# Performance work log

Measured on AMD Instinct MI355X. Metric: run time of the kernel, lower is better.

Reference implementation:

```python
import jax, jax.numpy as jnp
import numpy as np
from jax import lax

B, T, D, H, Z, L = 64, 1024, 128, 512, 64, 2

def lstm_layer(x_tbd, h0, c0, Wih, Whh, bih, bhh):
    # x_tbd: [T,B,Din]; precompute input contribution (big GEMM outside scan)
    gx = jnp.einsum('tbd,gd->tbg', x_tbd, Wih) + (bih + bhh)  # [T,B,4H]
    def step(carry, gxt):
        h, c = carry
        gates = gxt + h @ Whh.T
        i, f, g, o = jnp.split(gates, 4, axis=-1)
        c = jax.nn.sigmoid(f) * c + jax.nn.sigmoid(i) * jnp.tanh(g)
        h = jax.nn.sigmoid(o) * jnp.tanh(c)
        return (h, c), h
    (hT, cT), hs = lax.scan(step, (h0, c0), gx)
    return hs, hT, cT  # hs: [T,B,H]

def run_lstm(x_btd, h0_l, c0_l, params):
    # params: list of (Wih, Whh, bih, bhh) per layer; h0_l/c0_l: [L,B,H]
    seq = jnp.transpose(x_btd, (1, 0, 2))
    hTs = []
    for l, (Wih, Whh, bih, bhh) in enumerate(params):
        seq, hT, cT = lstm_layer(seq, h0_l[l], c0_l[l], Wih, Whh, bih, bhh)
        hTs.append(hT)
    return jnp.transpose(seq, (1, 0, 2)), jnp.stack(hTs)

def setup_inputs() -> dict:
    key = jax.random.key(0)
    ks = iter(jax.random.split(key, 32))
    s = 0.05
    d = {'x': jax.random.uniform(next(ks), (B, T, D), jnp.float32)}
    for pre in ('enc', 'dec'):
        for l in range(L):
            din = D if l == 0 else H
            d[f'{pre}_Wih{l}'] = jax.random.normal(next(ks), (4 * H, din), jnp.float32) * s
            d[f'{pre}_Whh{l}'] = jax.random.normal(next(ks), (4 * H, H), jnp.float32) * s
            d[f'{pre}_bih{l}'] = jnp.zeros((4 * H,), jnp.float32)
            d[f'{pre}_bhh{l}'] = jnp.zeros((4 * H,), jnp.float32)
    d['tl_W'] = jax.random.normal(next(ks), (Z, H), jnp.float32) * s
    d['tl_b'] = jnp.zeros((Z,), jnp.float32)
    d['lh_W'] = jax.random.normal(next(ks), (H * L, Z), jnp.float32) * s
    d['lh_b'] = jnp.zeros((H * L,), jnp.float32)
    d['op_W'] = jax.random.normal(next(ks), (D, H), jnp.float32) * s
    d['op_b'] = jnp.zeros((D,), jnp.float32)
    return d

def reference(x, enc_Wih0, enc_Whh0, enc_bih0, enc_bhh0, enc_Wih1, enc_Whh1, enc_bih1, enc_bhh1,
              dec_Wih0, dec_Whh0, dec_bih0, dec_bhh0, dec_Wih1, dec_Whh1, dec_bih1, dec_bhh1,
              tl_W, tl_b, lh_W, lh_b, op_W, op_b):
    enc_p = [(enc_Wih0, enc_Whh0, enc_bih0, enc_bhh0), (enc_Wih1, enc_Whh1, enc_bih1, enc_bhh1)]
    dec_p = [(dec_Wih0, dec_Whh0, dec_bih0, dec_bhh0), (dec_Wih1, dec_Whh1, dec_bih1, dec_bhh1)]
    zeros_lbh = jnp.zeros((L, B, H), x.dtype)
    # encode
    _, h_n = run_lstm(x, zeros_lbh, zeros_lbh, enc_p)
    z = h_n[-1] @ tl_W.T + tl_b  # [B,Z]
    # decode: zero input sequence, latent-derived initial hidden state
    init_h = jnp.tanh(z @ lh_W.T + lh_b).reshape(B, L, H).transpose(1, 0, 2)  # matches torch .view(L,B,H)? no
    init_h = jnp.tanh(z @ lh_W.T + lh_b).reshape(L, B, H)  # torch: view(num_layers, batch, hidden) on [B, H*L] flat -- faithful to source
    dec_in = jnp.zeros((B, T, D), x.dtype)
    dec_out, _ = run_lstm(dec_in, init_h, jnp.zeros_like(init_h), dec_p)
    recon = jax.nn.sigmoid(jnp.einsum('bth,dh->btd', dec_out, op_W) + op_b)
    return recon, z
```

## Files before the change

### kernel.cpp

```cpp
#include <hip/hip_runtime.h>
#include <cstdint>
#include <cstddef>

typedef unsigned short u16;
typedef unsigned int u32;
typedef __attribute__((ext_vector_type(8))) short short8;
typedef __attribute__((ext_vector_type(4))) float f32x4;

#define AGENT_SCOPE __HIP_MEMORY_SCOPE_AGENT
#define SPIN_CAP 20000000
#define POLL_CAP 200000
#define SENT 0xFFFFFFFFu

__device__ __forceinline__ u16 f2bf(float f) {
  u32 u = __float_as_uint(f);
  return (u16)((u + 0x7FFFu + ((u >> 16) & 1u)) >> 16);
}
__device__ __forceinline__ float bf2f(u16 s) { return __uint_as_float(((u32)s) << 16); }
__device__ __forceinline__ float sigm(float x) { return 1.f / (1.f + __expf(-x)); }
__device__ __forceinline__ float tanha(float x) { return 1.f - 2.f / (__expf(2.f * x) + 1.f); }
__device__ __forceinline__ void wait_vm0() { asm volatile("s_waitcnt vmcnt(0)" ::: "memory"); }

__global__ void __launch_bounds__(256, 1)
lstm_ae_kernel(const float* __restrict__ x,
    const float* __restrict__ eWih0, const float* __restrict__ eWhh0,
    const float* __restrict__ ebi0,  const float* __restrict__ ebh0,
    const float* __restrict__ eWih1, const float* __restrict__ eWhh1,
    const float* __restrict__ ebi1,  const float* __restrict__ ebh1,
    const float* __restrict__ dWhh0,
    const float* __restrict__ dbi0,  const float* __restrict__ dbh0,
    const float* __restrict__ dWih1, const float* __restrict__ dWhh1,
    const float* __restrict__ dbi1,  const float* __restrict__ dbh1,
    const float* __restrict__ tlW,   const float* __restrict__ tlb,
    const float* __restrict__ lhW,   const float* __restrict__ lhb,
    const float* __restrict__ opW,   const float* __restrict__ opb,
    float* __restrict__ out, char* __restrict__ wsb)
{
  __shared__ __align__(16) u16 sH0[16 * 520];
  __shared__ __align__(16) u16 sH1[16 * 520];
  __shared__ __align__(16) u16 sX[16 * 136];
  __shared__ __align__(16) u16 sOPW[2 * 520];
  __shared__ float sP[4 * 256];
  __shared__ float sBias[64];
  __shared__ float sC[256];
  __shared__ float sZ[16 * 64];
  __shared__ float sOPB[4];

  u32* gcnt  = (u32*)wsb;
  float* zbuf= (float*)(wsb + 4096);
  u32* h0r   = (u32*)(wsb + 32768);
  u32* h1r   = (u32*)(wsb + 229376);

  const int tid  = threadIdx.x;
  const int col  = blockIdx.x & 3;
  const int rowg = blockIdx.x >> 2;
  const int wid  = tid >> 6;
  const int lane = tid & 63;
  const int m    = lane & 15;
  const int qo   = (lane >> 4) * 8;

  auto stage_slot = [&](int q0, int q1, bool p0on, bool p1on) {
    const u32* b0 = h0r + ((q0 * 4 + col) << 12) + tid;
    const u32* b1 = h1r + ((q1 * 4 + col) << 12) + tid;
    u32 v0[16], v1[16];
    int it = 0; bool ok = false;
    while (!ok && it++ < POLL_CAP) {
      ok = true;
      if (p0on) {
        #pragma unroll
        for (int i = 0; i < 16; ++i) {
          v0[i] = __hip_atomic_load(b0 + i * 256, __ATOMIC_RELAXED, AGENT_SCOPE);
          ok &= (v0[i] != SENT);
        }
      }
      if (p1on) {
        #pragma unroll
        for (int i = 0; i < 16; ++i) {
          v1[i] = __hip_atomic_load(b1 + i * 256, __ATOMIC_RELAXED, AGENT_SCOPE);
          ok &= (v1[i] != SENT);
        }
      }
    }
    u32* dH0 = (u32*)sH0; u32* dH1 = (u32*)sH1;
    #pragma unroll
    for (int i = 0; i < 16; ++i) {
      int g = i * 256 + tid;
      int rg = g >> 6, b = (g >> 2) & 15, udw = g & 3;
      if (p0on) dH0[b * 260 + rg * 4 + udw] = v0[i];
      if (p1on) dH1[b * 260 + rg * 4 + udw] = v1[i];
    }
  };

  auto clears = [&](int s) {
    if (tid < 64) {
      int cq0 = (s + 1) % 3, cq1 = s % 3;
      __hip_atomic_store(h0r + ((cq0 * 4 + col) << 12) + (rowg << 6) + tid,
                         SENT, __ATOMIC_RELAXED, AGENT_SCOPE);
      __hip_atomic_store(h1r + ((cq1 * 4 + col) << 12) + (rowg << 6) + tid,
                         SENT, __ATOMIC_RELAXED, AGENT_SCOPE);
    }
  };

  auto stage_xt = [&](int s) {
    int b = tid >> 4, seg = tid & 15;
    const float* p = x + (size_t)(col * 16 + b) * 131072 + (size_t)s * 128 + seg * 8;
    float4 f0 = *(const float4*)p, f1 = *(const float4*)(p + 4);
    uint4 v;
    v.x = (u32)f2bf(f0.x) | ((u32)f2bf(f0.y) << 16);
    v.y = (u32)f2bf(f0.z) | ((u32)f2bf(f0.w) << 16);
    v.z = (u32)f2bf(f1.x) | ((u32)f2bf(f1.y) << 16);
    v.w = (u32)f2bf(f1.z) | ((u32)f2bf(f1.w) << 16);
    *(uint4*)(sX + b * 136 + seg * 8) = v;
  };

  auto ldw = [&](const float* W, int ld, int row, int kofs) -> short8 {
    const float* p = W + (size_t)row * ld + kofs + qo;
    float4 f0 = *(const float4*)p, f1 = *(const float4*)(p + 4);
    short8 r;
    r[0] = (short)f2bf(f0.x); r[1] = (short)f2bf(f0.y);
    r[2] = (short)f2bf(f0.z); r[3] = (short)f2bf(f0.w);
    r[4] = (short)f2bf(f1.x); r[5] = (short)f2bf(f1.y);
    r[6] = (short)f2bf(f1.z); r[7] = (short)f2bf(f1.w);
    return r;
  };

  auto act_store = [&](bool L0a, bool L1a, int q0, int q1) {
    int li = tid >> 7, b = (tid >> 3) & 15, u = tid & 7;
    bool actv = li ? L1a : L0a;
    float hv = 0.f;
    if (actv) {
      float gi = sP[(li*2)*256   + b*16 + u]     + sBias[li*32 + u];
      float gf = sP[(li*2)*256   + b*16 + 8 + u] + sBias[li*32 + 8 + u];
      float gg = sP[(li*2+1)*256 + b*16 + u]     + sBias[li*32 + 16 + u];
      float go = sP[(li*2+1)*256 + b*16 + 8 + u] + sBias[li*32 + 24 + u];
      float c = sC[(li*16 + b)*8 + u];
      c = sigm(gf)*c + sigm(gi)*tanha(gg);
      sC[(li*16 + b)*8 + u] = c;
      hv = sigm(go)*tanha(c);
    }
    u16 hb = f2bf(hv);
    u32 other = __shfl_xor((u32)hb, 1);
    if (actv && !(u & 1)) {
      u32 v = (u32)hb | (other << 16);
      u32* ring = li ? h1r : h0r;
      int q = li ? q1 : q0;
      __hip_atomic_store(ring + ((q * 4 + col) << 12) + (rowg << 6) + b * 4 + (u >> 1),
                         v, __ATOMIC_RELAXED, AGENT_SCOPE);
    }
  };

  auto gbar = [&](u32 target) {
    __syncthreads();
    if (tid == 0) {
      __hip_atomic_fetch_add(gcnt, 1u, __ATOMIC_RELEASE, AGENT_SCOPE);
      int it = 0;
      while (__hip_atomic_load(gcnt, __ATOMIC_RELAXED, AGENT_SCOPE) < target && ++it < SPIN_CAP) {}
      (void)__hip_atomic_load(gcnt, __ATOMIC_ACQUIRE, AGENT_SCOPE);
    }
    __syncthreads();
  };

  const int nl = (wid & 1) * 16 + m;
  const int gw = ((nl >> 3) << 9) + rowg * 8 + (nl & 7);

  short8 wb[32];

  if (wid < 2) {
    #pragma unroll
    for (int t = 0; t < 4; ++t)  wb[t]      = ldw(eWih0, 128, gw, t * 32);
    #pragma unroll
    for (int t = 0; t < 16; ++t) wb[4 + t]  = ldw(eWhh0, 512, gw, t * 32);
  } else {
    #pragma unroll
    for (int t = 0; t < 16; ++t) wb[t]      = ldw(eWih1, 512, gw, t * 32);
    #pragma unroll
    for (int t = 0; t < 16; ++t) wb[16 + t] = ldw(eWhh1, 512, gw, t * 32);
  }
  if (tid < 64) {
    int li = tid >> 5, n = tid & 31;
    int g = ((n >> 3) << 9) + rowg * 8 + (n & 7);
    sBias[li * 32 + n] = li ? (ebi1[g] + ebh1[g]) : (ebi0[g] + ebh0[g]);
  }
  sC[tid] = 0.f;
  __syncthreads();

  for (int s = 0; s <= 1024; ++s) {
    const bool L0 = (s < 1024), L1 = (s >= 1);
    if (L0) stage_xt(s);
    stage_slot((s + 2) % 3, (s + 1) % 3, true, s >= 1);
    __syncthreads();
    clears(s);

    f32x4 acc = {0.f, 0.f, 0.f, 0.f};
    if (wid < 2) {
      if (L0) {
        #pragma unroll
        for (int t = 0; t < 4; ++t) {
          short8 a = *(const short8*)(sX + m * 136 + t * 32 + qo);
          acc = __builtin_amdgcn_mfma_f32_16x16x32_bf16(a, wb[t], acc, 0, 0, 0);
        }
        #pragma unroll
        for (int t = 0; t < 16; ++t) {
          short8 a = *(const short8*)(sH0 + m * 520 + t * 32 + qo);
          acc = __builtin_amdgcn_mfma_f32_16x16x32_bf16(a, wb[4 + t], acc, 0, 0, 0);
        }
      }
    } else {
      if (L1) {
        #pragma unroll
        for (int t = 0; t < 16; ++t) {
          short8 a = *(const short8*)(sH0 + m * 520 + t * 32 + qo);
          acc = __builtin_amdgcn_mfma_f32_16x16x32_bf16(a, wb[t], acc, 0, 0, 0);
        }
        #pragma unroll
        for (int t = 0; t < 16; ++t) {
          short8 a = *(const short8*)(sH1 + m * 520 + t * 32 + qo);
          acc = __builtin_amdgcn_mfma_f32_16x16x32_bf16(a, wb[16 + t], acc, 0, 0, 0);
        }
      }
    }
    {
      bool wact = (wid < 2) ? L0 : L1;
      if (wact) {
        int mb = (lane >> 4) * 4;
        #pragma unroll
        for (int r = 0; r < 4; ++r) sP[wid * 256 + (mb + r) * 16 + m] = acc[r];
      }
    }
    __syncthreads();
    act_store(L0, L1, s % 3, (s + 2) % 3);
  }

  {
    const u32* b1 = h1r + ((0 * 4 + col) << 12) + tid;
    u32 v1[16];
    int it = 0; bool ok = false;
    while (!ok && it++ < POLL_CAP) {
      ok = true;
      #pragma unroll
      for (int i = 0; i < 16; ++i) {
        v1[i] = __hip_atomic_load(b1 + i * 256, __ATOMIC_RELAXED, AGENT_SCOPE);
        ok &= (v1[i] != SENT);
      }
    }
    u32* dH1 = (u32*)sH1;
    #pragma unroll
    for (int i = 0; i < 16; ++i) {
      int g = i * 256 + tid;
      dH1[((g >> 2) & 15) * 260 + (g >> 6) * 4 + (g & 3)] = v1[i];
    }
  }
  __syncthreads();
  if (tid < 16) {
    int b = tid;
    float acc = tlb[rowg];
    for (int kk = 0; kk < 512; kk += 8) {
      short8 hv = *(const short8*)(sH1 + b * 520 + kk);
      #pragma unroll
      for (int j = 0; j < 8; ++j) acc += bf2f((u16)hv[j]) * tlW[rowg * 512 + kk + j];
    }
    int gb = col * 16 + b;
    __hip_atomic_store((u32*)zbuf + gb * 64 + rowg, __float_as_uint(acc),
                       __ATOMIC_RELAXED, AGENT_SCOPE);
    out[8388608 + gb * 64 + rowg] = acc;
  }
  gbar(256);

  if (tid < 64) {
    #pragma unroll
    for (int q = 0; q < 3; ++q) {
      __hip_atomic_store(h0r + ((q * 4 + col) << 12) + (rowg << 6) + tid,
                         SENT, __ATOMIC_RELAXED, AGENT_SCOPE);
      __hip_atomic_store(h1r + ((q * 4 + col) << 12) + (rowg << 6) + tid,
                         SENT, __ATOMIC_RELAXED, AGENT_SCOPE);
    }
  }
  wait_vm0();

  if (wid < 2) {
    #pragma unroll
    for (int t = 0; t < 16; ++t) wb[t] = ldw(dWhh0, 512, gw, t * 32);
  } else {
    #pragma unroll
    for (int t = 0; t < 16; ++t) wb[t]      = ldw(dWih1, 512, gw, t * 32);
    #pragma unroll
    for (int t = 0; t < 16; ++t) wb[16 + t] = ldw(dWhh1, 512, gw, t * 32);
  }
  if (tid < 64) {
    int li = tid >> 5, n = tid & 31;
    int g = ((n >> 3) << 9) + rowg * 8 + (n & 7);
    sBias[li * 32 + n] = li ? (dbi1[g] + dbh1[g]) : (dbi0[g] + dbh0[g]);
  }
  for (int i = tid; i < 2 * 64; i += 256) {
    int dd = i >> 6, k = (i & 63) * 8;
    const float* p = opW + (size_t)(rowg * 2 + dd) * 512 + k;
    float4 f0 = *(const float4*)p, f1 = *(const float4*)(p + 4);
    uint4 v;
    v.x = (u32)f2bf(f0.x) | ((u32)f2bf(f0.y) << 16);
    v.y = (u32)f2bf(f0.z) | ((u32)f2bf(f0.w) << 16);
    v.z = (u32)f2bf(f1.x) | ((u32)f2bf(f1.y) << 16);
    v.w = (u32)f2bf(f1.z) | ((u32)f2bf(f1.w) << 16);
    *(uint4*)(sOPW + dd * 520 + k) = v;
  }
  if (tid < 2) sOPB[tid] = opb[rowg * 2 + tid];
  sC[tid] = 0.f;

  {
    int ri = tid >> 4, kk = (tid & 15) * 4;
    int zr = ((ri >> 3) << 5) + 8 * col + (ri & 7);
    #pragma unroll
    for (int j = 0; j < 4; ++j)
      sZ[ri * 64 + kk + j] = __uint_as_float(
          __hip_atomic_load((u32*)zbuf + zr * 64 + kk + j, __ATOMIC_RELAXED, AGENT_SCOPE));
  }
  __syncthreads();
  {
    int li = tid >> 7, hh = (tid >> 4) & 7, qb = (tid >> 3) & 1, u = tid & 7;
    int cc = qb * 512 + rowg * 8 + u;
    int bl = 2 * hh + qb;
    float acc2 = lhb[cc];
    const float* lw = lhW + (size_t)cc * 64;
    #pragma unroll 8
    for (int k = 0; k < 64; ++k) acc2 += sZ[(li * 8 + hh) * 64 + k] * lw[k];
    u16 hb = f2bf(tanha(acc2));
    u32 other = __shfl_xor((u32)hb, 1);
    if (!(u & 1)) {
      u32 v = (u32)hb | (other << 16);
      u32* ring = li ? h1r : h0r;
      __hip_atomic_store(ring + ((2 * 4 + col) << 12) + (rowg << 6) + bl * 4 + (u >> 1),
                         v, __ATOMIC_RELAXED, AGENT_SCOPE);
    }
  }
  gbar(512);

  for (int s = 0; s <= 1025; ++s) {
    const bool L0 = (s < 1024), L1 = (s >= 1 && s <= 1024), RC = (s >= 2);
    stage_slot((s + 2) % 3, (s + 1) % 3, s <= 1024, s >= 1);
    __syncthreads();
    clears(s);

    f32x4 acc = {0.f, 0.f, 0.f, 0.f};
    if (wid < 2) {
      if (L0) {
        #pragma unroll
        for (int t = 0; t < 16; ++t) {
          short8 a = *(const short8*)(sH0 + m * 520 + t * 32 + qo);
          acc = __builtin_amdgcn_mfma_f32_16x16x32_bf16(a, wb[t], acc, 0, 0, 0);
        }
      }
    } else {
      if (L1) {
        #pragma unroll
        for (int t = 0; t < 16; ++t) {
          short8 a = *(const short8*)(sH0 + m * 520 + t * 32 + qo);
          acc = __builtin_amdgcn_mfma_f32_16x16x32_bf16(a, wb[t], acc, 0, 0, 0);
        }
        #pragma unroll
        for (int t = 0; t < 16; ++t) {
          short8 a = *(const short8*)(sH1 + m * 520 + t * 32 + qo);
          acc = __builtin_amdgcn_mfma_f32_16x16x32_bf16(a, wb[16 + t], acc, 0, 0, 0);
        }
      }
    }
    {
      bool wact = (wid < 2) ? L0 : L1;
      if (wact) {
        int mb = (lane >> 4) * 4;
        #pragma unroll
        for (int r = 0; r < 4; ++r) sP[wid * 256 + (mb + r) * 16 + m] = acc[r];
      }
    }
    __syncthreads();
    act_store(L0, L1, s % 3, (s + 2) % 3);

    if (RC) {
      __syncthreads();
      int b = tid >> 4, dd = (tid >> 3) & 1, pt = tid & 7;
      float acc2 = 0.f;
      int k0 = pt * 64;
      for (int kk = 0; kk < 64; kk += 8) {
        short8 hv = *(const short8*)(sH1 + b * 520 + k0 + kk);
        short8 wv = *(const short8*)(sOPW + dd * 520 + k0 + kk);
        #pragma unroll
        for (int j = 0; j < 8; ++j) acc2 += bf2f((u16)hv[j]) * bf2f((u16)wv[j]);
      }
      sP[tid] = acc2;
      __syncthreads();
      if (tid < 32) {
        int b2 = tid >> 1, d2 = tid & 1;
        float sum = sOPB[d2];
        #pragma unroll
        for (int j = 0; j < 8; ++j) sum += sP[b2 * 16 + d2 * 8 + j];
        out[(size_t)(col * 16 + b2) * 131072 + (size_t)(s - 2) * 128 + rowg * 2 + d2]
            = sigm(sum);
      }
    }
  }
}

extern "C" void kernel_launch(void* const* d_in, const int* in_sizes, int n_in,
                              void* d_out, int out_size, void* d_ws, size_t ws_size,
                              hipStream_t stream) {
  (void)in_sizes; (void)n_in; (void)out_size; (void)ws_size;
  char* ws = (char*)d_ws;
  hipMemsetAsync(ws, 0, 32768, stream);
  hipMemsetAsync(ws + 32768, 0xFF, 131072, stream);
  hipMemsetAsync(ws + 163840, 0x00, 65536, stream);
  hipMemsetAsync(ws + 229376, 0xFF, 131072, stream);
  hipMemsetAsync(ws + 360448, 0x00, 65536, stream);
  lstm_ae_kernel<<<dim3(256), dim3(256), 0, stream>>>(
      (const float*)d_in[0],
      (const float*)d_in[1],  (const float*)d_in[2],
      (const float*)d_in[3],  (const float*)d_in[4],
      (const float*)d_in[5],  (const float*)d_in[6],
      (const float*)d_in[7],  (const float*)d_in[8],
      (const float*)d_in[10],
      (const float*)d_in[11], (const float*)d_in[12],
      (const float*)d_in[13], (const float*)d_in[14],
      (const float*)d_in[15], (const float*)d_in[16],
      (const float*)d_in[17], (const float*)d_in[18],
      (const float*)d_in[19], (const float*)d_in[20],
      (const float*)d_in[21], (const float*)d_in[22],
      (float*)d_out, (char*)d_ws);
}
```

Baseline: 6.444 ms.

## Balance MFMA work across waves, add per-column flags, move output projection to MFMA

Shifts part of layer-1's input-weight K range onto the layer-0 waves so all four waves issue a similar number of MFMAs per step. A second accumulator is reduced through extra sP slots. The scalar bf16 output-projection dot product and its extra barriers are replaced by MFMAs on the layer-0 waves using opW fragments held in registers. A per-block step flag with a wavefront ballot wait is added before ring polling, and staging of the next x timestep is moved after the activation. The risks are higher register pressure and the added flag polling traffic.

New measurement: 17.72 ms. 175% more time.

```diff
diff --git a/kernel.cpp b/kernel.cpp
--- a/kernel.cpp
+++ b/kernel.cpp
@@ -39,15 +39,15 @@
   __shared__ __align__(16) u16 sH0[16 * 520];
   __shared__ __align__(16) u16 sH1[16 * 520];
   __shared__ __align__(16) u16 sX[16 * 136];
-  __shared__ __align__(16) u16 sOPW[2 * 520];
-  __shared__ float sP[4 * 256];
+  __shared__ float sP[8 * 256];
   __shared__ float sBias[64];
   __shared__ float sC[256];
   __shared__ float sZ[16 * 64];
-  __shared__ float sOPB[4];
+  __shared__ float sOPB[2];
 
   u32* gcnt  = (u32*)wsb;
   float* zbuf= (float*)(wsb + 4096);
+  u32* flags = (u32*)(wsb + 24576);
   u32* h0r   = (u32*)(wsb + 32768);
   u32* h1r   = (u32*)(wsb + 229376);
 
@@ -58,6 +58,17 @@
   const int lane = tid & 63;
   const int m    = lane & 15;
   const int qo   = (lane >> 4) * 8;
+
+  u32* myflag = &flags[col * 64 + rowg];
+
+  auto flag_wait = [&](u32 target) {
+    const u32* fp = &flags[col * 64 + lane];
+    int it = 0;
+    while (it++ < POLL_CAP) {
+      u32 v = __hip_atomic_load(fp, __ATOMIC_RELAXED, AGENT_SCOPE);
+      if (__ballot(v >= target) == ~0ull) break;
+    }
+  };
 
   auto stage_slot = [&](int q0, int q1, bool p0on, bool p1on) {
     const u32* b0 = h0r + ((q0 * 4 + col) << 12) + tid;
@@ -124,15 +135,29 @@
     return r;
   };
 
+  auto spstore = [&](int slot, const f32x4& a) {
+    int mb = (lane >> 4) * 4;
+    #pragma unroll
+    for (int r = 0; r < 4; ++r) sP[slot * 256 + (mb + r) * 16 + m] = a[r];
+  };
+
   auto act_store = [&](bool L0a, bool L1a, int q0, int q1) {
     int li = tid >> 7, b = (tid >> 3) & 15, u = tid & 7;
     bool actv = li ? L1a : L0a;
     float hv = 0.f;
     if (actv) {
-      float gi = sP[(li*2)*256   + b*16 + u]     + sBias[li*32 + u];
-      float gf = sP[(li*2)*256   + b*16 + 8 + u] + sBias[li*32 + 8 + u];
-      float gg = sP[(li*2+1)*256 + b*16 + u]     + sBias[li*32 + 16 + u];
-      float go = sP[(li*2+1)*256 + b*16 + 8 + u] + sBias[li*32 + 24 + u];
+      float gi, gf, gg, go;
+      if (li == 0) {
+        gi = sP[0*256 + b*16 + u];       gf = sP[0*256 + b*16 + 8 + u];
+        gg = sP[1*256 + b*16 + u];       go = sP[1*256 + b*16 + 8 + u];
+      } else {
+        gi = sP[2*256 + b*16 + u]     + sP[4*256 + b*16 + u];
+        gf = sP[2*256 + b*16 + 8 + u] + sP[4*256 + b*16 + 8 + u];
+        gg = sP[3*256 + b*16 + u]     + sP[5*256 + b*16 + u];
+        go = sP[3*256 + b*16 + 8 + u] + sP[5*256 + b*16 + 8 + u];
+      }
+      gi += sBias[li*32 + u];      gf += sBias[li*32 + 8 + u];
+      gg += sBias[li*32 + 16 + u]; go += sBias[li*32 + 24 + u];
       float c = sC[(li*16 + b)*8 + u];
       c = sigm(gf)*c + sigm(gi)*tanha(gg);
       sC[(li*16 + b)*8 + u] = c;
@@ -163,18 +188,20 @@
   const int nl = (wid & 1) * 16 + m;
   const int gw = ((nl >> 3) << 9) + rowg * 8 + (nl & 7);
 
-  short8 wb[32];
+  short8 wb[28];
 
   if (wid < 2) {
     #pragma unroll
     for (int t = 0; t < 4; ++t)  wb[t]      = ldw(eWih0, 128, gw, t * 32);
     #pragma unroll
     for (int t = 0; t < 16; ++t) wb[4 + t]  = ldw(eWhh0, 512, gw, t * 32);
+    #pragma unroll
+    for (int t = 0; t < 6; ++t)  wb[20 + t] = ldw(eWih1, 512, gw, t * 32);
   } else {
     #pragma unroll
-    for (int t = 0; t < 16; ++t) wb[t]      = ldw(eWih1, 512, gw, t * 32);
-    #pragma unroll
-    for (int t = 0; t < 16; ++t) wb[16 + t] = ldw(eWhh1, 512, gw, t * 32);
+    for (int t = 0; t < 10; ++t) wb[t]      = ldw(eWih1, 512, gw, (6 + t) * 32);
+    #pragma unroll
+    for (int t = 0; t < 16; ++t) wb[10 + t] = ldw(eWhh1, 512, gw, t * 32);
   }
   if (tid < 64) {
     int li = tid >> 5, n = tid & 31;
@@ -182,55 +209,53 @@
     sBias[li * 32 + n] = li ? (ebi1[g] + ebh1[g]) : (ebi0[g] + ebh0[g]);
   }
   sC[tid] = 0.f;
+  stage_xt(0);
   __syncthreads();
 
   for (int s = 0; s <= 1024; ++s) {
     const bool L0 = (s < 1024), L1 = (s >= 1);
-    if (L0) stage_xt(s);
+    flag_wait((u32)s);
     stage_slot((s + 2) % 3, (s + 1) % 3, true, s >= 1);
     __syncthreads();
     clears(s);
 
-    f32x4 acc = {0.f, 0.f, 0.f, 0.f};
+    f32x4 accA = {0.f,0.f,0.f,0.f}, accB = {0.f,0.f,0.f,0.f};
     if (wid < 2) {
       if (L0) {
         #pragma unroll
         for (int t = 0; t < 4; ++t) {
           short8 a = *(const short8*)(sX + m * 136 + t * 32 + qo);
-          acc = __builtin_amdgcn_mfma_f32_16x16x32_bf16(a, wb[t], acc, 0, 0, 0);
+          accA = __builtin_amdgcn_mfma_f32_16x16x32_bf16(a, wb[t], accA, 0, 0, 0);
         }
-        #pragma unroll
-        for (int t = 0; t < 16; ++t) {
-          short8 a = *(const short8*)(sH0 + m * 520 + t * 32 + qo);
-          acc = __builtin_amdgcn_mfma_f32_16x16x32_bf16(a, wb[4 + t], acc, 0, 0, 0);
-        }
-      }
-    } else {
-      if (L1) {
-        #pragma unroll
-        for (int t = 0; t < 16; ++t) {
-          short8 a = *(const short8*)(sH0 + m * 520 + t * 32 + qo);
-          acc = __builtin_amdgcn_mfma_f32_16x16x32_bf16(a, wb[t], acc, 0, 0, 0);
-        }
-        #pragma unroll
-        for (int t = 0; t < 16; ++t) {
-          short8 a = *(const short8*)(sH1 + m * 520 + t * 32 + qo);
-          acc = __builtin_amdgcn_mfma_f32_16x16x32_bf16(a, wb[16 + t], acc, 0, 0, 0);
-        }
-      }
-    }
-    {
-      bool wact = (wid < 2) ? L0 : L1;
-      if (wact) {
-        int mb = (lane >> 4) * 4;
-        #pragma unroll
-        for (int r = 0; r < 4; ++r) sP[wid * 256 + (mb + r) * 16 + m] = acc[r];
-      }
-    }
+      }
+      #pragma unroll
+      for (int t = 0; t < 16; ++t) {
+        short8 a = *(const short8*)(sH0 + m * 520 + t * 32 + qo);
+        if (L0) accA = __builtin_amdgcn_mfma_f32_16x16x32_bf16(a, wb[4 + t], accA, 0, 0, 0);
+        if (L1 && t < 6) accB = __builtin_amdgcn_mfma_f32_16x16x32_bf16(a, wb[20 + t], accB, 0, 0, 0);
+      }
+    } else if (L1) {
+      #pragma unroll
+      for (int t = 0; t < 10; ++t) {
+        short8 a = *(const short8*)(sH0 + m * 520 + (6 + t) * 32 + qo);
+        accA = __builtin_amdgcn_mfma_f32_16x16x32_bf16(a, wb[t], accA, 0, 0, 0);
+      }
+      #pragma unroll
+      for (int t = 0; t < 16; ++t) {
+        short8 a = *(const short8*)(sH1 + m * 520 + t * 32 + qo);
+        accA = __builtin_amdgcn_mfma_f32_16x16x32_bf16(a, wb[10 + t], accA, 0, 0, 0);
+      }
+    }
+    if (wid < 2) { if (L0) spstore(wid, accA); if (L1) spstore(4 + wid, accB); }
+    else         { if (L1) spstore(wid, accA); }
     __syncthreads();
     act_store(L0, L1, s % 3, (s + 2) % 3);
-  }
-
+    if (s + 1 < 1024) stage_xt(s + 1);
+    if (tid == 0)
+      __hip_atomic_store(myflag, (u32)(s + 1), __ATOMIC_RELAXED, AGENT_SCOPE);
+  }
+
+  flag_wait(1025u);
   {
     const u32* b1 = h1r + ((0 * 4 + col) << 12) + tid;
     u32 v1[16];
@@ -275,32 +300,25 @@
                          SENT, __ATOMIC_RELAXED, AGENT_SCOPE);
     }
   }
-  wait_vm0();
 
   if (wid < 2) {
     #pragma unroll
-    for (int t = 0; t < 16; ++t) wb[t] = ldw(dWhh0, 512, gw, t * 32);
+    for (int t = 0; t < 16; ++t) wb[t]      = ldw(dWhh0, 512, gw, t * 32);
+    #pragma unroll
+    for (int t = 0; t < 4; ++t)  wb[16 + t] = ldw(dWih1, 512, gw, t * 32);
+    int rrow = rowg * 2 + (m < 2 ? m : 0);
+    #pragma unroll
+    for (int t = 0; t < 8; ++t)  wb[20 + t] = ldw(opW, 512, rrow, ((wid & 1) * 8 + t) * 32);
   } else {
     #pragma unroll
-    for (int t = 0; t < 16; ++t) wb[t]      = ldw(dWih1, 512, gw, t * 32);
-    #pragma unroll
-    for (int t = 0; t < 16; ++t) wb[16 + t] = ldw(dWhh1, 512, gw, t * 32);
+    for (int t = 0; t < 12; ++t) wb[t]      = ldw(dWih1, 512, gw, (4 + t) * 32);
+    #pragma unroll
+    for (int t = 0; t < 16; ++t) wb[12 + t] = ldw(dWhh1, 512, gw, t * 32);
   }
   if (tid < 64) {
     int li = tid >> 5, n = tid & 31;
     int g = ((n >> 3) << 9) + rowg * 8 + (n & 7);
     sBias[li * 32 + n] = li ? (dbi1[g] + dbh1[g]) : (dbi0[g] + dbh0[g]);
-  }
-  for (int i = tid; i < 2 * 64; i += 256) {
-    int dd = i >> 6, k = (i & 63) * 8;
-    const float* p = opW + (size_t)(rowg * 2 + dd) * 512 + k;
-    float4 f0 = *(const float4*)p, f1 = *(const float4*)(p + 4);
-    uint4 v;
-    v.x = (u32)f2bf(f0.x) | ((u32)f2bf(f0.y) << 16);
-    v.y = (u32)f2bf(f0.z) | ((u32)f2bf(f0.w) << 16);
-    v.z = (u32)f2bf(f1.x) | ((u32)f2bf(f1.y) << 16);
-    v.w = (u32)f2bf(f1.z) | ((u32)f2bf(f1.w) << 16);
-    *(uint4*)(sOPW + dd * 520 + k) = v;
   }
   if (tid < 2) sOPB[tid] = opb[rowg * 2 + tid];
   sC[tid] = 0.f;
@@ -335,66 +353,55 @@
 
   for (int s = 0; s <= 1025; ++s) {
     const bool L0 = (s < 1024), L1 = (s >= 1 && s <= 1024), RC = (s >= 2);
+    flag_wait((u32)(1025 + s));
     stage_slot((s + 2) % 3, (s + 1) % 3, s <= 1024, s >= 1);
     __syncthreads();
     clears(s);
 
-    f32x4 acc = {0.f, 0.f, 0.f, 0.f};
+    f32x4 accA = {0.f,0.f,0.f,0.f}, accB = {0.f,0.f,0.f,0.f}, accR = {0.f,0.f,0.f,0.f};
     if (wid < 2) {
-      if (L0) {
+      if (L0 || L1) {
         #pragma unroll
         for (int t = 0; t < 16; ++t) {
           short8 a = *(const short8*)(sH0 + m * 520 + t * 32 + qo);
-          acc = __builtin_amdgcn_mfma_f32_16x16x32_bf16(a, wb[t], acc, 0, 0, 0);
+          if (L0) accA = __builtin_amdgcn_mfma_f32_16x16x32_bf16(a, wb[t], accA, 0, 0, 0);
+          if (L1 && t < 4) accB = __builtin_amdgcn_mfma_f32_16x16x32_bf16(a, wb[16 + t], accB, 0, 0, 0);
         }
       }
-    } else {
-      if (L1) {
+      if (RC) {
         #pragma unroll
-        for (int t = 0; t < 16; ++t) {
-          short8 a = *(const short8*)(sH0 + m * 520 + t * 32 + qo);
-          acc = __builtin_amdgcn_mfma_f32_16x16x32_bf16(a, wb[t], acc, 0, 0, 0);
+        for (int t = 0; t < 8; ++t) {
+          short8 a = *(const short8*)(sH1 + m * 520 + ((wid & 1) * 8 + t) * 32 + qo);
+          accR = __builtin_amdgcn_mfma_f32_16x16x32_bf16(a, wb[20 + t], accR, 0, 0, 0);
         }
-        #pragma unroll
-        for (int t = 0; t < 16; ++t) {
-          short8 a = *(const short8*)(sH1 + m * 520 + t * 32 + qo);
-          acc = __builtin_amdgcn_mfma_f32_16x16x32_bf16(a, wb[16 + t], acc, 0, 0, 0);
-        }
-      }
-    }
-    {
-      bool wact = (wid < 2) ? L0 : L1;
-      if (wact) {
-        int mb = (lane >> 4) * 4;
-        #pragma unroll
-        for (int r = 0; r < 4; ++r) sP[wid * 256 + (mb + r) * 16 + m] = acc[r];
-      }
-    }
+      }
+    } else if (L1) {
+      #pragma unroll
+      for (int t = 0; t < 12; ++t) {
+        short8 a = *(const short8*)(sH0 + m * 520 + (4 + t) * 32 + qo);
+        accA = __builtin_amdgcn_mfma_f32_16x16x32_bf16(a, wb[t], accA, 0, 0, 0);
+      }
+      #pragma unroll
+      for (int t = 0; t < 16; ++t) {
+        short8 a = *(const short8*)(sH1 + m * 520 + t * 32 + qo);
+        accA = __builtin_amdgcn_mfma_f32_16x16x32_bf16(a, wb[12 + t], accA, 0, 0, 0);
+      }
+    }
+    if (wid < 2) {
+      if (L0) spstore(wid, accA);
+      if (L1) spstore(4 + wid, accB);
+      if (RC) spstore(6 + wid, accR);
+    } else if (L1) spstore(wid, accA);
     __syncthreads();
     act_store(L0, L1, s % 3, (s + 2) % 3);
-
-    if (RC) {
-      __syncthreads();
-      int b = tid >> 4, dd = (tid >> 3) & 1, pt = tid & 7;
-      float acc2 = 0.f;
-      int k0 = pt * 64;
-      for (int kk = 0; kk < 64; kk += 8) {
-        short8 hv = *(const short8*)(sH1 + b * 520 + k0 + kk);
-        short8 wv = *(const short8*)(sOPW + dd * 520 + k0 + kk);
-        #pragma unroll
-        for (int j = 0; j < 8; ++j) acc2 += bf2f((u16)hv[j]) * bf2f((u16)wv[j]);
-      }
-      sP[tid] = acc2;
-      __syncthreads();
-      if (tid < 32) {
-        int b2 = tid >> 1, d2 = tid & 1;
-        float sum = sOPB[d2];
-        #pragma unroll
-        for (int j = 0; j < 8; ++j) sum += sP[b2 * 16 + d2 * 8 + j];
-        out[(size_t)(col * 16 + b2) * 131072 + (size_t)(s - 2) * 128 + rowg * 2 + d2]
-            = sigm(sum);
-      }
-    }
+    if (RC && tid < 32) {
+      int b2 = tid >> 1, d2 = tid & 1;
+      float sum = sOPB[d2] + sP[6*256 + b2*16 + d2] + sP[7*256 + b2*16 + d2];
+      out[(size_t)(col * 16 + b2) * 131072 + (size_t)(s - 2) * 128 + rowg * 2 + d2]
+          = sigm(sum);
+    }
+    if (tid == 0)
+      __hip_atomic_store(myflag, (u32)(1026 + s), __ATOMIC_RELAXED, AGENT_SCOPE);
   }
 }
 
```
